# Optimization experiments

Measured on AMD Instinct MI355X. Metric: run time of the kernel, lower is better.

## Reference

```python
import jax, jax.numpy as jnp
import numpy as np

HEADS = 16  # per module init; all heads share the same weights -> identical outputs


def setup_inputs() -> dict:
    key = jax.random.key(0)
    k1, k2, k3, k4 = jax.random.split(key, 4)
    B, S, E, HD = 8, 2048, 1024, 64  # embed_size=1024, heads=16, head_dim=64
    x = jax.random.normal(k1, (B, S, E), dtype=jnp.float32)
    Wq = jax.random.normal(k2, (HD, E), dtype=jnp.float32) * (E ** -0.5)
    Wk = jax.random.normal(k3, (HD, E), dtype=jnp.float32) * (E ** -0.5)
    Wv = jax.random.normal(k4, (HD, E), dtype=jnp.float32) * (E ** -0.5)
    return {"x": x, "Wq": Wq, "Wk": Wk, "Wv": Wv}


def reference(x, Wq, Wk, Wv):
    # Linear(embed, head_dim, bias=False): y = x @ W.T
    q = jnp.einsum('bse,de->bsd', x, Wq)  # [B,S,64]
    k = jnp.einsum('bse,de->bsd', x, Wk)
    v = jnp.einsum('bse,de->bsd', x, Wv)
    # scores [b, i(query), k(key)] -- NO scaling (scaled_factor unused in source)
    scores = jnp.einsum('bij,bkj->bik', q, k)
    # nn.Softmax(dim=1): normalize over the QUERY axis (axis=1), faithful quirk
    attn = jax.nn.softmax(scores, axis=1)
    out = jnp.matmul(attn, v)  # [B,S,64]
    # Per-head loop reuses identical weights -> concat == tile across heads
    return jnp.tile(out, (1, 1, HEADS))  # [B,S,1024]
```

## Files before the change

kernel.cpp:

```cpp
#include <hip/hip_runtime.h>

#define BATCH 8
#define SEQ   2048
#define EMB   1024
#define HD    64
#define HEADS 16
#define BS    (BATCH * SEQ)
#define LOG2E 1.4426950408889634f

typedef _Float16 half8 __attribute__((ext_vector_type(8)));
typedef _Float16 half4 __attribute__((ext_vector_type(4)));
typedef float    f32x4 __attribute__((ext_vector_type(4)));

__device__ __forceinline__ float fexp2(float x) {
#if __has_builtin(__builtin_amdgcn_exp2f)
    return __builtin_amdgcn_exp2f(x);
#else
    return exp2f(x);
#endif
}

__device__ __forceinline__ float frcp(float x) {
#if __has_builtin(__builtin_amdgcn_rcpf)
    return __builtin_amdgcn_rcpf(x);
#else
    return 1.0f / x;
#endif
}

__device__ __forceinline__ void dma16(void* lds_base, const void* gsrc) {
    __builtin_amdgcn_global_load_lds(
        (const __attribute__((address_space(1))) unsigned int*)gsrc,
        (__attribute__((address_space(3))) unsigned int*)lds_base, 16, 0, 0);
}

__global__ __launch_bounds__(256) void wcvt_kernel(
    const float* __restrict__ Wq, const float* __restrict__ Wk,
    const float* __restrict__ Wv, _Float16* __restrict__ Wh)
{
    const int m = blockIdx.y;
    const float* src = (m == 0) ? Wq : (m == 1) ? Wk : Wv;
    const float scale = (m == 0) ? LOG2E : 1.0f;
    const int idx = (blockIdx.x * 256 + threadIdx.x) * 8;
    float4 f0 = *(const float4*)(src + idx);
    float4 f1 = *(const float4*)(src + idx + 4);
    half8 h;
    h[0] = (_Float16)(f0.x * scale); h[1] = (_Float16)(f0.y * scale);
    h[2] = (_Float16)(f0.z * scale); h[3] = (_Float16)(f0.w * scale);
    h[4] = (_Float16)(f1.x * scale); h[5] = (_Float16)(f1.y * scale);
    h[6] = (_Float16)(f1.z * scale); h[7] = (_Float16)(f1.w * scale);
    *(half8*)(Wh + (size_t)m * 65536 + idx) = h;
}

__global__ __launch_bounds__(512) void qkv_kernel(
    const float* __restrict__ x, const _Float16* __restrict__ Wh,
    _Float16* __restrict__ qh, _Float16* __restrict__ kh, _Float16* __restrict__ vpt)
{
    __shared__ __align__(16) char arena[65536];
    const int t = threadIdx.x, lane = t & 63, wave = t >> 6;
    const int l15 = lane & 15, quad = lane >> 4;
    const int strip = wave & 1, grp = wave >> 1;
    const int row0 = blockIdx.x * 32;

    auto issue = [&](int buf, int k0) {
        #pragma unroll
        for (int jj = 0; jj < 4; ++jj) {
            const int j = wave * 4 + jj;
            if (j < 8) {
                const int row = j * 4 + (lane >> 4);
                const int logi = (lane & 15) ^ (row & 15);
                dma16((float*)(arena + buf * 8192) + j * 256,
                      x + (size_t)(row0 + row) * EMB + k0 + logi * 4);
            } else {
                const int jw = j - 8;
                const int dd = jw * 8 + (lane >> 3);
                const int logi = (lane & 7) ^ (dd & 7);
                dma16((_Float16*)(arena + 16384 + buf * 24576) + jw * 512,
                      Wh + (size_t)(dd >> 6) * 65536 + (size_t)(dd & 63) * EMB
                         + k0 + logi * 8);
            }
        }
    };

    issue(0, 0);
    __syncthreads();

    f32x4 acc[3] = {};
    const int xrow = strip * 16 + l15;
    for (int it = 0; it < 16; ++it) {
        const int buf = it & 1;
        if (it + 1 < 16) issue(buf ^ 1, (it + 1) * 64);
        const float* xb = (const float*)(arena + buf * 8192);
        const _Float16* wb = (const _Float16*)(arena + 16384 + buf * 24576);
        half8 a[2];
        #pragma unroll
        for (int kc = 0; kc < 2; ++kc) {
            const int s0 = kc * 8 + quad * 2;
            f32x4 u0 = *(const f32x4*)(xb + xrow * 64 + ((s0    ) ^ (l15 & 15)) * 4);
            f32x4 u1 = *(const f32x4*)(xb + xrow * 64 + ((s0 + 1) ^ (l15 & 15)) * 4);
            a[kc][0] = (_Float16)u0[0]; a[kc][1] = (_Float16)u0[1];
            a[kc][2] = (_Float16)u0[2]; a[kc][3] = (_Float16)u0[3];
            a[kc][4] = (_Float16)u1[0]; a[kc][5] = (_Float16)u1[1];
            a[kc][6] = (_Float16)u1[2]; a[kc][7] = (_Float16)u1[3];
        }
        #pragma unroll
        for (int j = 0; j < 3; ++j) {
            const int dd = (grp * 3 + j) * 16 + l15;
            #pragma unroll
            for (int kc = 0; kc < 2; ++kc) {
                half8 bfr = *(const half8*)(wb + dd * 64
                              + (((kc * 4 + quad) ^ (l15 & 7)) * 8));
                acc[j] = __builtin_amdgcn_mfma_f32_16x16x32_f16(a[kc], bfr, acc[j], 0, 0, 0);
            }
        }
        __syncthreads();
    }

    #pragma unroll
    for (int j = 0; j < 3; ++j) {
        const int c = grp * 3 + j, m = c >> 2, n = c & 3;
        if (m < 2) {
            _Float16* __restrict__ dst = (m == 0) ? qh : kh;
            #pragma unroll
            for (int r = 0; r < 4; ++r)
                dst[(size_t)(row0 + strip * 16 + quad * 4 + r) * HD + n * 16 + l15] =
                    (_Float16)acc[j][r];
        } else {
            const int rg = row0 + strip * 16 + quad * 4;
            const int b = rg >> 11, s = rg & 2047;
            half4 h;
            h[0] = (_Float16)acc[j][0]; h[1] = (_Float16)acc[j][1];
            h[2] = (_Float16)acc[j][2]; h[3] = (_Float16)acc[j][3];
            *(half4*)(vpt + ((size_t)b * HD + n * 16 + l15) * SEQ + s) = h;
        }
    }
}

__global__ __launch_bounds__(256) void stats_kernel(
    const _Float16* __restrict__ qh, const _Float16* __restrict__ kh,
    float* __restrict__ l_part)
{
    __shared__ __align__(16) char arena[16384];
    __shared__ float red[4][32];
    const int t = threadIdx.x, lane = t & 63, wave = t >> 6;
    const int l15 = lane & 15, quad = lane >> 4;
    const int b = blockIdx.y, c0 = blockIdx.x * 32, z = blockIdx.z;
    const int qbase = z * 1024;

    half8 ka[2][2];
    #pragma unroll
    for (int kt = 0; kt < 2; ++kt) {
        const _Float16* kp = kh + ((size_t)b * SEQ + c0 + kt * 16 + l15) * HD + quad * 8;
        ka[kt][0] = *(const half8*)(kp);
        ka[kt][1] = *(const half8*)(kp + 32);
    }

    auto issue = [&](int buf, int q0) {
        #pragma unroll
        for (int jj = 0; jj < 2; ++jj) {
            const int j = wave * 2 + jj;
            const int qq = j * 8 + (lane >> 3);
            const int logi = (lane & 7) ^ (qq & 7);
            dma16((_Float16*)(arena + buf * 8192) + j * 512,
                  qh + ((size_t)b * SEQ + q0 + qq) * HD + logi * 8);
        }
    };

    issue(0, qbase);
    __syncthreads();

    float csum[2][4] = {};
    const int qrow = wave * 16 + l15;
    for (int it = 0; it < 16; ++it) {
        const int buf = it & 1;
        if (it + 1 < 16) issue(buf ^ 1, qbase + (it + 1) * 64);
        const _Float16* qb = (const _Float16*)(arena + buf * 8192);
        half8 bq[2];
        #pragma unroll
        for (int kc = 0; kc < 2; ++kc)
            bq[kc] = *(const half8*)(qb + qrow * 64
                        + (((kc * 4 + quad) ^ (l15 & 7)) * 8));
        f32x4 s0 = {}, s1 = {};
        s0 = __builtin_amdgcn_mfma_f32_16x16x32_f16(ka[0][0], bq[0], s0, 0, 0, 0);
        s0 = __builtin_amdgcn_mfma_f32_16x16x32_f16(ka[0][1], bq[1], s0, 0, 0, 0);
        s1 = __builtin_amdgcn_mfma_f32_16x16x32_f16(ka[1][0], bq[0], s1, 0, 0, 0);
        s1 = __builtin_amdgcn_mfma_f32_16x16x32_f16(ka[1][1], bq[1], s1, 0, 0, 0);
        #pragma unroll
        for (int r = 0; r < 4; ++r) {
            csum[0][r] += fexp2(s0[r]);
            csum[1][r] += fexp2(s1[r]);
        }
        __syncthreads();
    }
    #pragma unroll
    for (int kt = 0; kt < 2; ++kt)
        #pragma unroll
        for (int r = 0; r < 4; ++r) {
            csum[kt][r] += __shfl_xor(csum[kt][r], 1);
            csum[kt][r] += __shfl_xor(csum[kt][r], 2);
            csum[kt][r] += __shfl_xor(csum[kt][r], 4);
            csum[kt][r] += __shfl_xor(csum[kt][r], 8);
        }
    if (l15 == 0) {
        #pragma unroll
        for (int kt = 0; kt < 2; ++kt)
            #pragma unroll
            for (int r = 0; r < 4; ++r)
                red[wave][kt * 16 + quad * 4 + r] = csum[kt][r];
    }
    __syncthreads();
    if (t < 32)
        l_part[(size_t)z * BS + (size_t)b * SEQ + c0 + t] =
            red[0][t] + red[1][t] + red[2][t] + red[3][t];
}

__global__ __launch_bounds__(256) void out_kernel(
    const _Float16* __restrict__ qh, const _Float16* __restrict__ kh,
    const _Float16* __restrict__ vpt, const float* __restrict__ l_part,
    float* __restrict__ opart)
{
    __shared__ __align__(16) char arena[37888];
    const int t = threadIdx.x, lane = t & 63, wave = t >> 6;
    const int l15 = lane & 15, quad = lane >> 4;
    const int rw = wave & 1, kw = wave >> 1;
    const int b = blockIdx.y, r0 = blockIdx.x * 32, z = blockIdx.z;
    const int kbase = z * 1024;

    half8 aq[2];
    {
        const _Float16* qp = qh + ((size_t)b * SEQ + r0 + rw * 16 + l15) * HD + quad * 8;
        aq[0] = *(const half8*)(qp);
        aq[1] = *(const half8*)(qp + 32);
    }

    auto issue = [&](int buf, int c0) {
        #pragma unroll
        for (int jj = 0; jj < 4; ++jj) {
            if (wave < 2) {
                const int j = wave * 4 + jj;
                const int key = j * 8 + (lane >> 3);
                const int logi = (lane & 7) ^ (key & 7);
                dma16((_Float16*)(arena + buf * 8192) + j * 512,
                      kh + ((size_t)b * SEQ + c0 + key) * HD + logi * 8);
            } else {
                const int j = (wave - 2) * 4 + jj;
                const int d = j * 8 + (lane >> 3);
                const int logi = (lane & 7) ^ (d & 7);
                dma16((_Float16*)(arena + 16384 + buf * 8192) + j * 512,
                      vpt + ((size_t)b * HD + d) * SEQ + c0 + logi * 8);
            }
        }
    };

    const float* lp = l_part + (size_t)b * SEQ;
    float lnxt[2][2];
    auto loadl = [&](int c0, float (&dst)[2][2]) {
        #pragma unroll
        for (int ct = 0; ct < 2; ++ct) {
            const int kg = c0 + kw * 32 + ct * 16 + l15;
            dst[ct][0] = lp[kg];
            dst[ct][1] = lp[BS + kg];
        }
    };

    issue(0, kbase);
    loadl(kbase, lnxt);
    __syncthreads();

    _Float16* psb = (_Float16*)(arena + 32768) + wave * 640;
    f32x4 oacc[4] = {};
    for (int it = 0; it < 16; ++it) {
        const int buf = it & 1;
        float lc[2][2];
        lc[0][0] = lnxt[0][0]; lc[0][1] = lnxt[0][1];
        lc[1][0] = lnxt[1][0]; lc[1][1] = lnxt[1][1];
        if (it + 1 < 16) {
            issue(buf ^ 1, kbase + (it + 1) * 64);
            loadl(kbase + (it + 1) * 64, lnxt);
        }
        const _Float16* kb = (const _Float16*)(arena + buf * 8192);
        const _Float16* vb = (const _Float16*)(arena + 16384 + buf * 8192);

        f32x4 s[2] = {};
        #pragma unroll
        for (int ct = 0; ct < 2; ++ct) {
            const int key = kw * 32 + ct * 16 + l15;
            #pragma unroll
            for (int kc = 0; kc < 2; ++kc) {
                half8 kf = *(const half8*)(kb + key * 64
                             + (((kc * 4 + quad) ^ (l15 & 7)) * 8));
                s[ct] = __builtin_amdgcn_mfma_f32_16x16x32_f16(aq[kc], kf, s[ct], 0, 0, 0);
            }
        }
        #pragma unroll
        for (int ct = 0; ct < 2; ++ct) {
            const float li = frcp(lc[ct][0] + lc[ct][1]);
            #pragma unroll
            for (int r = 0; r < 4; ++r)
                psb[(quad * 4 + r) * 40 + ct * 16 + l15] =
                    (_Float16)(fexp2(s[ct][r]) * li);
        }
        half8 pa = *(const half8*)(psb + l15 * 40 + quad * 8);
        #pragma unroll
        for (int n = 0; n < 4; ++n) {
            const int d = n * 16 + l15;
            half8 vf = *(const half8*)(vb + d * 64
                         + (((kw * 4 + quad) ^ (l15 & 7)) * 8));
            oacc[n] = __builtin_amdgcn_mfma_f32_16x16x32_f16(pa, vf, oacc[n], 0, 0, 0);
        }
        __syncthreads();
    }

    float* red = (float*)(arena);
    float* fin = (float*)(arena + 8704);
    if (kw == 1) {
        #pragma unroll
        for (int n = 0; n < 4; ++n)
            #pragma unroll
            for (int r = 0; r < 4; ++r)
                red[(rw * 16 + quad * 4 + r) * 68 + n * 16 + l15] = oacc[n][r];
    }
    __syncthreads();
    if (kw == 0) {
        #pragma unroll
        for (int n = 0; n < 4; ++n)
            #pragma unroll
            for (int r = 0; r < 4; ++r)
                fin[(rw * 16 + quad * 4 + r) * 68 + n * 16 + l15] =
                    oacc[n][r] + red[(rw * 16 + quad * 4 + r) * 68 + n * 16 + l15];
    }
    __syncthreads();

    const int row = t >> 3, s8 = t & 7;
    float4 u0 = *(float4*)(fin + row * 68 + s8 * 8);
    float4 u1 = *(float4*)(fin + row * 68 + s8 * 8 + 4);
    float* dst = opart + (size_t)z * ((size_t)BS * HD)
               + ((size_t)b * SEQ + r0 + row) * HD + s8 * 8;
    *(float4*)(dst)     = u0;
    *(float4*)(dst + 4) = u1;
}

__global__ __launch_bounds__(256) void bcast_kernel(
    const float* __restrict__ opart, float* __restrict__ out)
{
    const int row = blockIdx.x;
    const int t = threadIdx.x;
    const int d = (t * 4) & 63;
    const float* o0 = opart + (size_t)row * HD + d;
    const float* o1 = o0 + (size_t)BS * HD;
    float4 a = *(const float4*)o0;
    float4 c = *(const float4*)o1;
    float4 s;
    s.x = a.x + c.x; s.y = a.y + c.y; s.z = a.z + c.z; s.w = a.w + c.w;
    *(float4*)(out + (size_t)row * (HD * HEADS) + t * 4) = s;
}

extern "C" void kernel_launch(void* const* d_in, const int* in_sizes, int n_in,
                              void* d_out, int out_size, void* d_ws, size_t ws_size,
                              hipStream_t stream)
{
    const float* x  = (const float*)d_in[0];
    const float* Wq = (const float*)d_in[1];
    const float* Wk = (const float*)d_in[2];
    const float* Wv = (const float*)d_in[3];
    float* out = (float*)d_out;

    const size_t N = (size_t)BATCH * SEQ * HD;
    _Float16* qh  = (_Float16*)d_ws;
    _Float16* kh  = qh + N;
    _Float16* vpt = kh + N;
    _Float16* Wh  = vpt + N;
    float* l_part = (float*)(Wh + 196608);
    float* opart  = l_part + 2 * BS;

    wcvt_kernel <<<dim3(32, 3),    256, 0, stream>>>(Wq, Wk, Wv, Wh);
    qkv_kernel  <<<dim3(512),      512, 0, stream>>>(x, Wh, qh, kh, vpt);
    stats_kernel<<<dim3(64, 8, 2), 256, 0, stream>>>(qh, kh, l_part);
    out_kernel  <<<dim3(64, 8, 2), 256, 0, stream>>>(qh, kh, vpt, l_part, opart);
    bcast_kernel<<<dim3(BS),       256, 0, stream>>>(opart, out);
}
```

Before: 170.0 us.

## Shrink LDS staging: direct global loads for W, Q, K, V operands

The QKV projection kernel moves to 16-row blocks of 256 threads. Only x is staged through a small double-buffered LDS arena, and the fp16 weights are loaded straight into registers with a manual ping-pong prefetch. The stats and output kernels stop staging Q, K and V tiles in LDS and instead read MFMA operands directly from global memory (relying on cache), which removes the per-iteration barriers. The intent is higher occupancy (launch_bounds min 4 blocks) and less synchronisation. The cost is uncoalesced or redundant global reads, for example the transposed V reads per lane, and less latency hiding for those loads.

```diff
diff --git a/kernel.cpp b/kernel.cpp
--- a/kernel.cpp
+++ b/kernel.cpp
@@ -52,52 +52,42 @@
     *(half8*)(Wh + (size_t)m * 65536 + idx) = h;
 }
 
-__global__ __launch_bounds__(512) void qkv_kernel(
+__global__ __launch_bounds__(256, 4) void qkv_kernel(
     const float* __restrict__ x, const _Float16* __restrict__ Wh,
     _Float16* __restrict__ qh, _Float16* __restrict__ kh, _Float16* __restrict__ vpt)
 {
-    __shared__ __align__(16) char arena[65536];
+    __shared__ __align__(16) char arena[8192];
     const int t = threadIdx.x, lane = t & 63, wave = t >> 6;
     const int l15 = lane & 15, quad = lane >> 4;
-    const int strip = wave & 1, grp = wave >> 1;
-    const int row0 = blockIdx.x * 32;
+    const int grp = wave;
+    const int row0 = blockIdx.x * 16;
 
     auto issue = [&](int buf, int k0) {
-        #pragma unroll
-        for (int jj = 0; jj < 4; ++jj) {
-            const int j = wave * 4 + jj;
-            if (j < 8) {
-                const int row = j * 4 + (lane >> 4);
-                const int logi = (lane & 15) ^ (row & 15);
-                dma16((float*)(arena + buf * 8192) + j * 256,
-                      x + (size_t)(row0 + row) * EMB + k0 + logi * 4);
-            } else {
-                const int jw = j - 8;
-                const int dd = jw * 8 + (lane >> 3);
-                const int logi = (lane & 7) ^ (dd & 7);
-                dma16((_Float16*)(arena + 16384 + buf * 24576) + jw * 512,
-                      Wh + (size_t)(dd >> 6) * 65536 + (size_t)(dd & 63) * EMB
-                         + k0 + logi * 8);
-            }
-        }
+        const int row = wave * 4 + (lane >> 4);
+        const int logi = (lane & 15) ^ (row & 15);
+        dma16((float*)(arena + buf * 4096) + wave * 256,
+              x + (size_t)(row0 + row) * EMB + k0 + logi * 4);
     };
-
-    issue(0, 0);
-    __syncthreads();
+    auto loadW = [&](int k0, half8 (&w)[3][2]) {
+        #pragma unroll
+        for (int j = 0; j < 3; ++j) {
+            const int g = (grp * 3 + j) * 16 + l15;
+            const _Float16* wp = Wh + (size_t)(g >> 6) * 65536
+                               + (size_t)(g & 63) * EMB + k0 + quad * 8;
+            w[j][0] = *(const half8*)(wp);
+            w[j][1] = *(const half8*)(wp + 32);
+        }
+    };
 
     f32x4 acc[3] = {};
-    const int xrow = strip * 16 + l15;
-    for (int it = 0; it < 16; ++it) {
-        const int buf = it & 1;
-        if (it + 1 < 16) issue(buf ^ 1, (it + 1) * 64);
-        const float* xb = (const float*)(arena + buf * 8192);
-        const _Float16* wb = (const _Float16*)(arena + 16384 + buf * 24576);
+    auto step = [&](int buf, const half8 (&w)[3][2]) {
+        const float* xb = (const float*)(arena + buf * 4096);
         half8 a[2];
         #pragma unroll
         for (int kc = 0; kc < 2; ++kc) {
             const int s0 = kc * 8 + quad * 2;
-            f32x4 u0 = *(const f32x4*)(xb + xrow * 64 + ((s0    ) ^ (l15 & 15)) * 4);
-            f32x4 u1 = *(const f32x4*)(xb + xrow * 64 + ((s0 + 1) ^ (l15 & 15)) * 4);
+            f32x4 u0 = *(const f32x4*)(xb + l15 * 64 + ((s0    ) ^ l15) * 4);
+            f32x4 u1 = *(const f32x4*)(xb + l15 * 64 + ((s0 + 1) ^ l15) * 4);
             a[kc][0] = (_Float16)u0[0]; a[kc][1] = (_Float16)u0[1];
             a[kc][2] = (_Float16)u0[2]; a[kc][3] = (_Float16)u0[3];
             a[kc][4] = (_Float16)u1[0]; a[kc][5] = (_Float16)u1[1];
@@ -105,14 +95,22 @@
         }
         #pragma unroll
         for (int j = 0; j < 3; ++j) {
-            const int dd = (grp * 3 + j) * 16 + l15;
-            #pragma unroll
-            for (int kc = 0; kc < 2; ++kc) {
-                half8 bfr = *(const half8*)(wb + dd * 64
-                              + (((kc * 4 + quad) ^ (l15 & 7)) * 8));
-                acc[j] = __builtin_amdgcn_mfma_f32_16x16x32_f16(a[kc], bfr, acc[j], 0, 0, 0);
-            }
-        }
+            acc[j] = __builtin_amdgcn_mfma_f32_16x16x32_f16(a[0], w[j][0], acc[j], 0, 0, 0);
+            acc[j] = __builtin_amdgcn_mfma_f32_16x16x32_f16(a[1], w[j][1], acc[j], 0, 0, 0);
+        }
+    };
+
+    half8 wA[3][2], wB[3][2];
+    issue(0, 0);
+    loadW(0, wA);
+    __syncthreads();
+    for (int it = 0; it < 16; it += 2) {
+        issue(1, (it + 1) * 64);
+        loadW((it + 1) * 64, wB);
+        step(0, wA);
+        __syncthreads();
+        if (it + 2 < 16) { issue(0, (it + 2) * 64); loadW((it + 2) * 64, wA); }
+        step(1, wB);
         __syncthreads();
     }
 
@@ -123,10 +121,10 @@
             _Float16* __restrict__ dst = (m == 0) ? qh : kh;
             #pragma unroll
             for (int r = 0; r < 4; ++r)
-                dst[(size_t)(row0 + strip * 16 + quad * 4 + r) * HD + n * 16 + l15] =
+                dst[(size_t)(row0 + quad * 4 + r) * HD + n * 16 + l15] =
                     (_Float16)acc[j][r];
         } else {
-            const int rg = row0 + strip * 16 + quad * 4;
+            const int rg = row0 + quad * 4;
             const int b = rg >> 11, s = rg & 2047;
             half4 h;
             h[0] = (_Float16)acc[j][0]; h[1] = (_Float16)acc[j][1];
@@ -136,16 +134,14 @@
     }
 }
 
-__global__ __launch_bounds__(256) void stats_kernel(
+__global__ __launch_bounds__(256, 4) void stats_kernel(
     const _Float16* __restrict__ qh, const _Float16* __restrict__ kh,
     float* __restrict__ l_part)
 {
-    __shared__ __align__(16) char arena[16384];
     __shared__ float red[4][32];
     const int t = threadIdx.x, lane = t & 63, wave = t >> 6;
     const int l15 = lane & 15, quad = lane >> 4;
     const int b = blockIdx.y, c0 = blockIdx.x * 32, z = blockIdx.z;
-    const int qbase = z * 1024;
 
     half8 ka[2][2];
     #pragma unroll
@@ -155,42 +151,22 @@
         ka[kt][1] = *(const half8*)(kp + 32);
     }
 
-    auto issue = [&](int buf, int q0) {
-        #pragma unroll
-        for (int jj = 0; jj < 2; ++jj) {
-            const int j = wave * 2 + jj;
-            const int qq = j * 8 + (lane >> 3);
-            const int logi = (lane & 7) ^ (qq & 7);
-            dma16((_Float16*)(arena + buf * 8192) + j * 512,
-                  qh + ((size_t)b * SEQ + q0 + qq) * HD + logi * 8);
-        }
-    };
-
-    issue(0, qbase);
-    __syncthreads();
-
+    const _Float16* qp0 = qh + ((size_t)b * SEQ + z * 1024 + wave * 16 + l15) * HD + quad * 8;
     float csum[2][4] = {};
-    const int qrow = wave * 16 + l15;
     for (int it = 0; it < 16; ++it) {
-        const int buf = it & 1;
-        if (it + 1 < 16) issue(buf ^ 1, qbase + (it + 1) * 64);
-        const _Float16* qb = (const _Float16*)(arena + buf * 8192);
-        half8 bq[2];
-        #pragma unroll
-        for (int kc = 0; kc < 2; ++kc)
-            bq[kc] = *(const half8*)(qb + qrow * 64
-                        + (((kc * 4 + quad) ^ (l15 & 7)) * 8));
+        const _Float16* qp = qp0 + (size_t)it * 64 * HD;
+        half8 bq0 = *(const half8*)(qp);
+        half8 bq1 = *(const half8*)(qp + 32);
         f32x4 s0 = {}, s1 = {};
-        s0 = __builtin_amdgcn_mfma_f32_16x16x32_f16(ka[0][0], bq[0], s0, 0, 0, 0);
-        s0 = __builtin_amdgcn_mfma_f32_16x16x32_f16(ka[0][1], bq[1], s0, 0, 0, 0);
-        s1 = __builtin_amdgcn_mfma_f32_16x16x32_f16(ka[1][0], bq[0], s1, 0, 0, 0);
-        s1 = __builtin_amdgcn_mfma_f32_16x16x32_f16(ka[1][1], bq[1], s1, 0, 0, 0);
+        s0 = __builtin_amdgcn_mfma_f32_16x16x32_f16(ka[0][0], bq0, s0, 0, 0, 0);
+        s0 = __builtin_amdgcn_mfma_f32_16x16x32_f16(ka[0][1], bq1, s0, 0, 0, 0);
+        s1 = __builtin_amdgcn_mfma_f32_16x16x32_f16(ka[1][0], bq0, s1, 0, 0, 0);
+        s1 = __builtin_amdgcn_mfma_f32_16x16x32_f16(ka[1][1], bq1, s1, 0, 0, 0);
         #pragma unroll
         for (int r = 0; r < 4; ++r) {
             csum[0][r] += fexp2(s0[r]);
             csum[1][r] += fexp2(s1[r]);
         }
-        __syncthreads();
     }
     #pragma unroll
     for (int kt = 0; kt < 2; ++kt)
@@ -214,12 +190,12 @@
             red[0][t] + red[1][t] + red[2][t] + red[3][t];
 }
 
-__global__ __launch_bounds__(256) void out_kernel(
+__global__ __launch_bounds__(256, 4) void out_kernel(
     const _Float16* __restrict__ qh, const _Float16* __restrict__ kh,
     const _Float16* __restrict__ vpt, const float* __restrict__ l_part,
     float* __restrict__ opart)
 {
-    __shared__ __align__(16) char arena[37888];
+    __shared__ __align__(16) char arena[22528];
     const int t = threadIdx.x, lane = t & 63, wave = t >> 6;
     const int l15 = lane & 15, quad = lane >> 4;
     const int rw = wave & 1, kw = wave >> 1;
@@ -233,86 +209,41 @@
         aq[1] = *(const half8*)(qp + 32);
     }
 
-    auto issue = [&](int buf, int c0) {
-        #pragma unroll
-        for (int jj = 0; jj < 4; ++jj) {
-            if (wave < 2) {
-                const int j = wave * 4 + jj;
-                const int key = j * 8 + (lane >> 3);
-                const int logi = (lane & 7) ^ (key & 7);
-                dma16((_Float16*)(arena + buf * 8192) + j * 512,
-                      kh + ((size_t)b * SEQ + c0 + key) * HD + logi * 8);
-            } else {
-                const int j = (wave - 2) * 4 + jj;
-                const int d = j * 8 + (lane >> 3);
-                const int logi = (lane & 7) ^ (d & 7);
-                dma16((_Float16*)(arena + 16384 + buf * 8192) + j * 512,
-                      vpt + ((size_t)b * HD + d) * SEQ + c0 + logi * 8);
-            }
-        }
-    };
-
     const float* lp = l_part + (size_t)b * SEQ;
-    float lnxt[2][2];
-    auto loadl = [&](int c0, float (&dst)[2][2]) {
-        #pragma unroll
-        for (int ct = 0; ct < 2; ++ct) {
-            const int kg = c0 + kw * 32 + ct * 16 + l15;
-            dst[ct][0] = lp[kg];
-            dst[ct][1] = lp[BS + kg];
-        }
-    };
-
-    issue(0, kbase);
-    loadl(kbase, lnxt);
-    __syncthreads();
-
-    _Float16* psb = (_Float16*)(arena + 32768) + wave * 640;
+    _Float16* psb = (_Float16*)(arena) + wave * 640;
     f32x4 oacc[4] = {};
     for (int it = 0; it < 16; ++it) {
-        const int buf = it & 1;
-        float lc[2][2];
-        lc[0][0] = lnxt[0][0]; lc[0][1] = lnxt[0][1];
-        lc[1][0] = lnxt[1][0]; lc[1][1] = lnxt[1][1];
-        if (it + 1 < 16) {
-            issue(buf ^ 1, kbase + (it + 1) * 64);
-            loadl(kbase + (it + 1) * 64, lnxt);
-        }
-        const _Float16* kb = (const _Float16*)(arena + buf * 8192);
-        const _Float16* vb = (const _Float16*)(arena + 16384 + buf * 8192);
-
+        const int c0 = kbase + it * 64;
         f32x4 s[2] = {};
+        float li[2];
         #pragma unroll
         for (int ct = 0; ct < 2; ++ct) {
-            const int key = kw * 32 + ct * 16 + l15;
-            #pragma unroll
-            for (int kc = 0; kc < 2; ++kc) {
-                half8 kf = *(const half8*)(kb + key * 64
-                             + (((kc * 4 + quad) ^ (l15 & 7)) * 8));
-                s[ct] = __builtin_amdgcn_mfma_f32_16x16x32_f16(aq[kc], kf, s[ct], 0, 0, 0);
-            }
-        }
-        #pragma unroll
-        for (int ct = 0; ct < 2; ++ct) {
-            const float li = frcp(lc[ct][0] + lc[ct][1]);
+            const int key = c0 + kw * 32 + ct * 16 + l15;
+            const _Float16* kp = kh + ((size_t)b * SEQ + key) * HD + quad * 8;
+            half8 kf0 = *(const half8*)(kp);
+            half8 kf1 = *(const half8*)(kp + 32);
+            s[ct] = __builtin_amdgcn_mfma_f32_16x16x32_f16(aq[0], kf0, s[ct], 0, 0, 0);
+            s[ct] = __builtin_amdgcn_mfma_f32_16x16x32_f16(aq[1], kf1, s[ct], 0, 0, 0);
+            li[ct] = frcp(lp[key] + lp[BS + key]);
+        }
+        #pragma unroll
+        for (int ct = 0; ct < 2; ++ct)
             #pragma unroll
             for (int r = 0; r < 4; ++r)
                 psb[(quad * 4 + r) * 40 + ct * 16 + l15] =
-                    (_Float16)(fexp2(s[ct][r]) * li);
-        }
+                    (_Float16)(fexp2(s[ct][r]) * li[ct]);
         half8 pa = *(const half8*)(psb + l15 * 40 + quad * 8);
         #pragma unroll
         for (int n = 0; n < 4; ++n) {
             const int d = n * 16 + l15;
-            half8 vf = *(const half8*)(vb + d * 64
-                         + (((kw * 4 + quad) ^ (l15 & 7)) * 8));
+            half8 vf = *(const half8*)(vpt + ((size_t)b * HD + d) * SEQ
+                                       + c0 + (kw * 4 + quad) * 8);
             oacc[n] = __builtin_amdgcn_mfma_f32_16x16x32_f16(pa, vf, oacc[n], 0, 0, 0);
         }
-        __syncthreads();
-    }
-
-    float* red = (float*)(arena);
-    float* fin = (float*)(arena + 8704);
+    }
+
+    float* red = (float*)(arena + 5120);
+    float* fin = (float*)(arena + 13824);
     if (kw == 1) {
         #pragma unroll
         for (int n = 0; n < 4; ++n)
@@ -374,7 +305,7 @@
     float* opart  = l_part + 2 * BS;
 
     wcvt_kernel <<<dim3(32, 3),    256, 0, stream>>>(Wq, Wk, Wv, Wh);
-    qkv_kernel  <<<dim3(512),      512, 0, stream>>>(x, Wh, qh, kh, vpt);
+    qkv_kernel  <<<dim3(1024),     256, 0, stream>>>(x, Wh, qh, kh, vpt);
     stats_kernel<<<dim3(64, 8, 2), 256, 0, stream>>>(qh, kh, l_part);
     out_kernel  <<<dim3(64, 8, 2), 256, 0, stream>>>(qh, kh, vpt, l_part, opart);
     bcast_kernel<<<dim3(BS),       256, 0, stream>>>(opart, out);
```

New measurement: 240.3 us. 41.3% more time.

## Double per-block tile to 64 rows/keys and drop intra-block key-split reduction

Applied to the files above, without the earlier changes.

Stats and out kernels now each handle 64 keys or query rows per block instead of 32, halving the grid. In out_kernel each wave owns 16 query rows and processes all 64 keys per tile, which removes the split-K LDS reduction and writes accumulators straight to global memory. Each staged K/V/Q tile is therefore reused across twice as many rows. The l_part values are now read directly inside the loop rather than prefetched one iteration ahead. The trade-offs are fewer blocks (512) for occupancy, a larger LDS footprint, and uncoalesced scalar stores to opart.

```diff
diff --git a/kernel.cpp b/kernel.cpp
--- a/kernel.cpp
+++ b/kernel.cpp
@@ -141,15 +141,15 @@
     float* __restrict__ l_part)
 {
     __shared__ __align__(16) char arena[16384];
-    __shared__ float red[4][32];
+    __shared__ float red[4][64];
     const int t = threadIdx.x, lane = t & 63, wave = t >> 6;
     const int l15 = lane & 15, quad = lane >> 4;
-    const int b = blockIdx.y, c0 = blockIdx.x * 32, z = blockIdx.z;
+    const int b = blockIdx.y, c0 = blockIdx.x * 64, z = blockIdx.z;
     const int qbase = z * 1024;
 
-    half8 ka[2][2];
+    half8 ka[4][2];
     #pragma unroll
-    for (int kt = 0; kt < 2; ++kt) {
+    for (int kt = 0; kt < 4; ++kt) {
         const _Float16* kp = kh + ((size_t)b * SEQ + c0 + kt * 16 + l15) * HD + quad * 8;
         ka[kt][0] = *(const half8*)(kp);
         ka[kt][1] = *(const half8*)(kp + 32);
@@ -169,31 +169,27 @@
     issue(0, qbase);
     __syncthreads();
 
-    float csum[2][4] = {};
+    float csum[4][4] = {};
     const int qrow = wave * 16 + l15;
     for (int it = 0; it < 16; ++it) {
         const int buf = it & 1;
         if (it + 1 < 16) issue(buf ^ 1, qbase + (it + 1) * 64);
         const _Float16* qb = (const _Float16*)(arena + buf * 8192);
-        half8 bq[2];
-        #pragma unroll
-        for (int kc = 0; kc < 2; ++kc)
-            bq[kc] = *(const half8*)(qb + qrow * 64
-                        + (((kc * 4 + quad) ^ (l15 & 7)) * 8));
-        f32x4 s0 = {}, s1 = {};
-        s0 = __builtin_amdgcn_mfma_f32_16x16x32_f16(ka[0][0], bq[0], s0, 0, 0, 0);
-        s0 = __builtin_amdgcn_mfma_f32_16x16x32_f16(ka[0][1], bq[1], s0, 0, 0, 0);
-        s1 = __builtin_amdgcn_mfma_f32_16x16x32_f16(ka[1][0], bq[0], s1, 0, 0, 0);
-        s1 = __builtin_amdgcn_mfma_f32_16x16x32_f16(ka[1][1], bq[1], s1, 0, 0, 0);
-        #pragma unroll
-        for (int r = 0; r < 4; ++r) {
-            csum[0][r] += fexp2(s0[r]);
-            csum[1][r] += fexp2(s1[r]);
+        half8 bq0 = *(const half8*)(qb + qrow * 64 + (((quad    ) ^ (l15 & 7)) * 8));
+        half8 bq1 = *(const half8*)(qb + qrow * 64 + (((4 + quad) ^ (l15 & 7)) * 8));
+        #pragma unroll
+        for (int kt = 0; kt < 4; ++kt) {
+            f32x4 s = {};
+            s = __builtin_amdgcn_mfma_f32_16x16x32_f16(ka[kt][0], bq0, s, 0, 0, 0);
+            s = __builtin_amdgcn_mfma_f32_16x16x32_f16(ka[kt][1], bq1, s, 0, 0, 0);
+            #pragma unroll
+            for (int r = 0; r < 4; ++r)
+                csum[kt][r] += fexp2(s[r]);
         }
         __syncthreads();
     }
     #pragma unroll
-    for (int kt = 0; kt < 2; ++kt)
+    for (int kt = 0; kt < 4; ++kt)
         #pragma unroll
         for (int r = 0; r < 4; ++r) {
             csum[kt][r] += __shfl_xor(csum[kt][r], 1);
@@ -203,13 +199,13 @@
         }
     if (l15 == 0) {
         #pragma unroll
-        for (int kt = 0; kt < 2; ++kt)
+        for (int kt = 0; kt < 4; ++kt)
             #pragma unroll
             for (int r = 0; r < 4; ++r)
                 red[wave][kt * 16 + quad * 4 + r] = csum[kt][r];
     }
     __syncthreads();
-    if (t < 32)
+    if (t < 64)
         l_part[(size_t)z * BS + (size_t)b * SEQ + c0 + t] =
             red[0][t] + red[1][t] + red[2][t] + red[3][t];
 }
@@ -219,16 +215,15 @@
     const _Float16* __restrict__ vpt, const float* __restrict__ l_part,
     float* __restrict__ opart)
 {
-    __shared__ __align__(16) char arena[37888];
+    __shared__ __align__(16) char arena[42496];
     const int t = threadIdx.x, lane = t & 63, wave = t >> 6;
     const int l15 = lane & 15, quad = lane >> 4;
-    const int rw = wave & 1, kw = wave >> 1;
-    const int b = blockIdx.y, r0 = blockIdx.x * 32, z = blockIdx.z;
+    const int b = blockIdx.y, r0 = blockIdx.x * 64, z = blockIdx.z;
     const int kbase = z * 1024;
 
     half8 aq[2];
     {
-        const _Float16* qp = qh + ((size_t)b * SEQ + r0 + rw * 16 + l15) * HD + quad * 8;
+        const _Float16* qp = qh + ((size_t)b * SEQ + r0 + wave * 16 + l15) * HD + quad * 8;
         aq[0] = *(const half8*)(qp);
         aq[1] = *(const half8*)(qp + 32);
     }
@@ -253,91 +248,54 @@
     };
 
     const float* lp = l_part + (size_t)b * SEQ;
-    float lnxt[2][2];
-    auto loadl = [&](int c0, float (&dst)[2][2]) {
-        #pragma unroll
-        for (int ct = 0; ct < 2; ++ct) {
-            const int kg = c0 + kw * 32 + ct * 16 + l15;
-            dst[ct][0] = lp[kg];
-            dst[ct][1] = lp[BS + kg];
-        }
-    };
 
     issue(0, kbase);
-    loadl(kbase, lnxt);
     __syncthreads();
 
-    _Float16* psb = (_Float16*)(arena + 32768) + wave * 640;
+    _Float16* psb = (_Float16*)(arena + 32768) + wave * 1216;
     f32x4 oacc[4] = {};
     for (int it = 0; it < 16; ++it) {
         const int buf = it & 1;
-        float lc[2][2];
-        lc[0][0] = lnxt[0][0]; lc[0][1] = lnxt[0][1];
-        lc[1][0] = lnxt[1][0]; lc[1][1] = lnxt[1][1];
-        if (it + 1 < 16) {
-            issue(buf ^ 1, kbase + (it + 1) * 64);
-            loadl(kbase + (it + 1) * 64, lnxt);
-        }
+        if (it + 1 < 16) issue(buf ^ 1, kbase + (it + 1) * 64);
         const _Float16* kb = (const _Float16*)(arena + buf * 8192);
         const _Float16* vb = (const _Float16*)(arena + 16384 + buf * 8192);
 
-        f32x4 s[2] = {};
-        #pragma unroll
-        for (int ct = 0; ct < 2; ++ct) {
-            const int key = kw * 32 + ct * 16 + l15;
-            #pragma unroll
-            for (int kc = 0; kc < 2; ++kc) {
-                half8 kf = *(const half8*)(kb + key * 64
-                             + (((kc * 4 + quad) ^ (l15 & 7)) * 8));
-                s[ct] = __builtin_amdgcn_mfma_f32_16x16x32_f16(aq[kc], kf, s[ct], 0, 0, 0);
-            }
-        }
-        #pragma unroll
-        for (int ct = 0; ct < 2; ++ct) {
-            const float li = frcp(lc[ct][0] + lc[ct][1]);
+        #pragma unroll
+        for (int ct = 0; ct < 4; ++ct) {
+            const int key = ct * 16 + l15;
+            f32x4 s = {};
+            half8 kf0 = *(const half8*)(kb + key * 64 + (((quad    ) ^ (l15 & 7)) * 8));
+            half8 kf1 = *(const half8*)(kb + key * 64 + (((4 + quad) ^ (l15 & 7)) * 8));
+            s = __builtin_amdgcn_mfma_f32_16x16x32_f16(aq[0], kf0, s, 0, 0, 0);
+            s = __builtin_amdgcn_mfma_f32_16x16x32_f16(aq[1], kf1, s, 0, 0, 0);
+            const int kg = kbase + it * 64 + key;
+            const float li = frcp(lp[kg] + lp[BS + kg]);
             #pragma unroll
             for (int r = 0; r < 4; ++r)
-                psb[(quad * 4 + r) * 40 + ct * 16 + l15] =
-                    (_Float16)(fexp2(s[ct][r]) * li);
-        }
-        half8 pa = *(const half8*)(psb + l15 * 40 + quad * 8);
+                psb[(quad * 4 + r) * 76 + ct * 16 + l15] =
+                    (_Float16)(fexp2(s[r]) * li);
+        }
+        half8 paA = *(const half8*)(psb + l15 * 76 + quad * 8);
+        half8 paB = *(const half8*)(psb + l15 * 76 + 32 + quad * 8);
         #pragma unroll
         for (int n = 0; n < 4; ++n) {
             const int d = n * 16 + l15;
-            half8 vf = *(const half8*)(vb + d * 64
-                         + (((kw * 4 + quad) ^ (l15 & 7)) * 8));
-            oacc[n] = __builtin_amdgcn_mfma_f32_16x16x32_f16(pa, vf, oacc[n], 0, 0, 0);
+            half8 vfA = *(const half8*)(vb + d * 64 + (((quad    ) ^ (l15 & 7)) * 8));
+            half8 vfB = *(const half8*)(vb + d * 64 + (((4 + quad) ^ (l15 & 7)) * 8));
+            oacc[n] = __builtin_amdgcn_mfma_f32_16x16x32_f16(paA, vfA, oacc[n], 0, 0, 0);
+            oacc[n] = __builtin_amdgcn_mfma_f32_16x16x32_f16(paB, vfB, oacc[n], 0, 0, 0);
         }
         __syncthreads();
     }
 
-    float* red = (float*)(arena);
-    float* fin = (float*)(arena + 8704);
-    if (kw == 1) {
-        #pragma unroll
-        for (int n = 0; n < 4; ++n)
-            #pragma unroll
-            for (int r = 0; r < 4; ++r)
-                red[(rw * 16 + quad * 4 + r) * 68 + n * 16 + l15] = oacc[n][r];
-    }
-    __syncthreads();
-    if (kw == 0) {
-        #pragma unroll
-        for (int n = 0; n < 4; ++n)
-            #pragma unroll
-            for (int r = 0; r < 4; ++r)
-                fin[(rw * 16 + quad * 4 + r) * 68 + n * 16 + l15] =
-                    oacc[n][r] + red[(rw * 16 + quad * 4 + r) * 68 + n * 16 + l15];
-    }
-    __syncthreads();
-
-    const int row = t >> 3, s8 = t & 7;
-    float4 u0 = *(float4*)(fin + row * 68 + s8 * 8);
-    float4 u1 = *(float4*)(fin + row * 68 + s8 * 8 + 4);
-    float* dst = opart + (size_t)z * ((size_t)BS * HD)
-               + ((size_t)b * SEQ + r0 + row) * HD + s8 * 8;
-    *(float4*)(dst)     = u0;
-    *(float4*)(dst + 4) = u1;
+    #pragma unroll
+    for (int n = 0; n < 4; ++n)
+        #pragma unroll
+        for (int r = 0; r < 4; ++r) {
+            const int row = r0 + wave * 16 + quad * 4 + r;
+            opart[(size_t)z * ((size_t)BS * HD)
+                  + ((size_t)b * SEQ + row) * HD + n * 16 + l15] = oacc[n][r];
+        }
 }
 
 __global__ __launch_bounds__(256) void bcast_kernel(
@@ -375,7 +333,7 @@
 
     wcvt_kernel <<<dim3(32, 3),    256, 0, stream>>>(Wq, Wk, Wv, Wh);
     qkv_kernel  <<<dim3(512),      512, 0, stream>>>(x, Wh, qh, kh, vpt);
-    stats_kernel<<<dim3(64, 8, 2), 256, 0, stream>>>(qh, kh, l_part);
-    out_kernel  <<<dim3(64, 8, 2), 256, 0, stream>>>(qh, kh, vpt, l_part, opart);
+    stats_kernel<<<dim3(32, 8, 2), 256, 0, stream>>>(qh, kh, l_part);
+    out_kernel  <<<dim3(32, 8, 2), 256, 0, stream>>>(qh, kh, vpt, l_part, opart);
     bcast_kernel<<<dim3(BS),       256, 0, stream>>>(opart, out);
 }
```

Result: slower. 174.8 us (+2.8%).
